# Kernel tuning notes

Hardware: AMD Instinct MI355X
Metric: run time of the kernel (lower is better)

The kernel has to match this reference:

```python
import jax, jax.numpy as jnp
import numpy as np

N_NODES = 50000
N_EDGES = 800000
F_IN = 128
HID = 256
K = 5
N_GRAPHS = 64


def setup_inputs() -> dict:
    key = jax.random.key(0)
    ks = jax.random.split(key, 16)
    x = jax.random.normal(ks[0], (N_NODES, F_IN), dtype=jnp.float32)
    edge_index = jax.random.randint(ks[1], (2, N_EDGES), 0, N_NODES, dtype=jnp.int32)
    edge_weight = jax.random.uniform(ks[2], (N_EDGES,), dtype=jnp.float32)
    batch = jnp.sort(jax.random.randint(ks[3], (N_NODES,), 0, N_GRAPHS, dtype=jnp.int32))
    s = 0.05
    W1 = jax.random.normal(ks[4], (K, F_IN, HID), dtype=jnp.float32) * s
    b1 = jnp.zeros((HID,), dtype=jnp.float32)
    W2 = jax.random.normal(ks[5], (K, HID, HID), dtype=jnp.float32) * s
    b2 = jnp.zeros((HID,), dtype=jnp.float32)
    W3 = jax.random.normal(ks[6], (K, HID, HID), dtype=jnp.float32) * s
    b3 = jnp.zeros((HID,), dtype=jnp.float32)
    lw1 = jax.random.normal(ks[7], (HID, HID), dtype=jnp.float32) * s
    lb1 = jnp.zeros((HID,), dtype=jnp.float32)
    lw2 = jax.random.normal(ks[8], (HID, 1), dtype=jnp.float32) * s
    lb2 = jnp.zeros((1,), dtype=jnp.float32)
    return dict(x=x, edge_index=edge_index, edge_weight=edge_weight, batch=batch,
                W1=W1, b1=b1, W2=W2, b2=b2, W3=W3, b3=b3,
                lw1=lw1, lb1=lb1, lw2=lw2, lb2=lb2)


def _lap_weights(edge_index, edge_weight, num_nodes):
    # PyG ChebConv with normalization='sym', lambda_max=2.0:
    # L_hat = 2*L/lambda_max - I = -D^{-1/2} A D^{-1/2} on the off-diagonal,
    # zero diagonal. Degree via scatter on edge_index[0].
    src, dst = edge_index[0], edge_index[1]
    deg = jax.ops.segment_sum(edge_weight, src, num_segments=num_nodes)
    dis = jnp.where(deg > 0, jax.lax.rsqrt(jnp.maximum(deg, 1e-30)), 0.0)
    return -(dis[src] * edge_weight * dis[dst])


def _cheb_conv(x, src, dst, lap_w, W, b):
    # propagate: gather from src, weight, scatter-add to dst
    n = x.shape[0]
    prop = lambda z: jax.ops.segment_sum(lap_w[:, None] * z[src], dst, num_segments=n)
    Tx0 = x
    out = Tx0 @ W[0]
    Tx1 = prop(x)
    out = out + Tx1 @ W[1]
    for k in range(2, W.shape[0]):
        Tx2 = 2.0 * prop(Tx1) - Tx0
        out = out + Tx2 @ W[k]
        Tx0, Tx1 = Tx1, Tx2
    return out + b


def reference(x, edge_index, edge_weight, batch, W1, b1, W2, b2, W3, b3, lw1, lb1, lw2, lb2):
    src, dst = edge_index[0], edge_index[1]
    lap_w = _lap_weights(edge_index, edge_weight, x.shape[0])
    h = jax.nn.relu(_cheb_conv(x, src, dst, lap_w, W1, b1))
    h = _cheb_conv(h, src, dst, lap_w, W2, b2)
    h = jax.nn.relu(_cheb_conv(h, src, dst, lap_w, W3, b3))
    # global mean pool over graphs in the batch
    sums = jax.ops.segment_sum(h, batch, num_segments=N_GRAPHS)
    cnts = jax.ops.segment_sum(jnp.ones((h.shape[0],), h.dtype), batch, num_segments=N_GRAPHS)
    g = sums / jnp.maximum(cnts, 1.0)[:, None]
    g = jax.nn.relu(g)  # dropout is identity in eval mode
    g = g @ lw1 + lb1
    g = g @ lw2 + lb2
    return jax.nn.sigmoid(g)
```

## Files before the change

### kernel.cpp

```cpp
#include <hip/hip_runtime.h>
#include <math.h>

typedef unsigned int uint;
typedef unsigned short ushort;
typedef __bf16 bf16x8 __attribute__((ext_vector_type(8)));
typedef float f32x4 __attribute__((ext_vector_type(4)));
typedef __attribute__((address_space(1))) const void gvoid;
typedef __attribute__((address_space(3))) void svoid;

__device__ __forceinline__ float b2f(ushort u) {
  uint v = ((uint)u) << 16;
  return __uint_as_float(v);
}
__device__ __forceinline__ ushort f2b(float f) {
  uint u = __float_as_uint(f);
  u += 0x7FFFu + ((u >> 16) & 1u);
  return (ushort)(u >> 16);
}
__device__ __forceinline__ uint pack2(float a, float b) {
  return (uint)f2b(a) | ((uint)f2b(b) << 16);
}


__global__ void edge_kernel(const int* __restrict__ src, const int* __restrict__ dst,
                            const float* __restrict__ w, float* __restrict__ degp,
                            int* __restrict__ cntp, int ne, int nb) {
  int e = blockIdx.x * blockDim.x + threadIdx.x;
  if (e < ne) {
    int part = blockIdx.x & 7;
    atomicAdd(&degp[(size_t)part * nb + src[e]], w[e]);
    atomicAdd(&cntp[(size_t)part * nb + dst[e]], 1);
  }
}

__global__ __launch_bounds__(256) void node_kernel(const float* __restrict__ degp,
                                                   const int* __restrict__ cntp,
                                                   float* __restrict__ dis,
                                                   int* __restrict__ rowstart,
                                                   int* __restrict__ rowcnt,
                                                   int* __restrict__ cursor,
                                                   int* __restrict__ total,
                                                   const int* __restrict__ batch,
                                                   int nb, int ng, int* __restrict__ bnd) {
  __shared__ int ls[256];
  __shared__ int base;
  int tid = threadIdx.x;
  int i = blockIdx.x * 256 + tid;
  int c = 0;
  float d = 0.f;
  if (i < nb) {
#pragma unroll
    for (int p = 0; p < 8; ++p) {
      c += cntp[(size_t)p * nb + i];
      d += degp[(size_t)p * nb + i];
    }
  }
  ls[tid] = c;
  __syncthreads();
  for (int off = 1; off < 256; off <<= 1) {
    int v = (tid >= off) ? ls[tid - off] : 0;
    __syncthreads();
    ls[tid] += v;
    __syncthreads();
  }
  if (tid == 255) base = atomicAdd(total, ls[255]);
  __syncthreads();
  if (i < nb) {
    int pos = base + ls[tid] - c;
    rowstart[i] = pos;
    cursor[i] = pos;
    rowcnt[i] = c;
    dis[i] = d > 0.f ? rsqrtf(fmaxf(d, 1e-30f)) : 0.f;
  }
  if (blockIdx.x == 0 && tid <= ng) {
    int lo = 0, hi = nb;
    while (lo < hi) {
      int mid = (lo + hi) >> 1;
      if (batch[mid] < tid) lo = mid + 1; else hi = mid;
    }
    bnd[tid] = lo;
  }
}

__global__ void scatter_kernel(const int* __restrict__ src, const int* __restrict__ dst,
                               const float* __restrict__ w, const float* __restrict__ dis,
                               int* __restrict__ cursor, int2* __restrict__ cv, int ne) {
  int e = blockIdx.x * blockDim.x + threadIdx.x;
  if (e < ne) {
    int d = dst[e], s = src[e];
    int pos = atomicAdd(&cursor[d], 1);
    float v = -(dis[s] * w[e] * dis[d]);
    cv[pos] = make_int2(s, __float_as_int(v));
  }
}


__global__ void xcvt_kernel(const float* __restrict__ x, uint* __restrict__ o, int total) {
  int i = blockIdx.x * blockDim.x + threadIdx.x;
  if (i < total) {
    float2 v = *(const float2*)(x + (size_t)i * 2);
    o[i] = pack2(v.x, v.y);
  }
}

__global__ void wprep_kernel(const float* __restrict__ W, ushort* __restrict__ WT,
                             int shift, int Ktot, int total) {
  int id = blockIdx.x * blockDim.x + threadIdx.x;
  if (id >= total) return;
  int n = id / Ktot;
  int k = id - n * Ktot;
  int fin = k & ((1 << shift) - 1);
  int ord = k >> shift;
  WT[id] = f2b(W[(size_t)(ord << shift) * 256 + (size_t)fin * 256 + n]);
}

__global__ void wprep2_kernel(const float* __restrict__ W2, ushort* __restrict__ WT2,
                              const float* __restrict__ W3, ushort* __restrict__ WT3,
                              int tot) {
  int id = blockIdx.x * blockDim.x + threadIdx.x;
  if (id >= 2 * tot) return;
  const float* W = (id < tot) ? W2 : W3;
  ushort* WT = (id < tot) ? WT2 : WT3;
  int t = (id < tot) ? id : id - tot;
  int n = t / 1280;
  int k = t - n * 1280;
  int fin = k & 255;
  int ord = k >> 8;
  WT[t] = f2b(W[(size_t)(ord << 8) * 256 + (size_t)fin * 256 + n]);
}


#define RFL __builtin_amdgcn_readfirstlane

template <int WIDE>
__global__ __launch_bounds__(256) void spmm_wave(const int* __restrict__ rowstart,
                                                 const int* __restrict__ rowcnt,
                                                 const int2* __restrict__ cv,
                                                 const uint* __restrict__ X,
                                                 uint* __restrict__ out,
                                                 const uint* __restrict__ sub,
                                                 float alpha, int nb) {
  int row = blockIdx.x * 4 + (threadIdx.x >> 6);
  if (row >= nb) return;
  int lane = threadIdx.x & 63;
  int e0 = RFL(rowstart[row]);
  int cnt = RFL(rowcnt[row]);
  int e1 = e0 + cnt;
  float a0 = 0.f, a1 = 0.f, a2 = 0.f, a3 = 0.f;
  int e = e0;
  if (WIDE) {
    const uint2* Xr = (const uint2*)X;
    for (; e + 4 <= e1; e += 4) {
      int2 p0 = cv[e], p1 = cv[e + 1], p2 = cv[e + 2], p3 = cv[e + 3];
      int c0 = RFL(p0.x); float v0 = __uint_as_float(RFL((uint)p0.y));
      int c1 = RFL(p1.x); float v1 = __uint_as_float(RFL((uint)p1.y));
      int c2 = RFL(p2.x); float v2 = __uint_as_float(RFL((uint)p2.y));
      int c3 = RFL(p3.x); float v3 = __uint_as_float(RFL((uint)p3.y));
      uint2 g0 = Xr[(size_t)c0 * 64 + lane];
      uint2 g1 = Xr[(size_t)c1 * 64 + lane];
      uint2 g2 = Xr[(size_t)c2 * 64 + lane];
      uint2 g3 = Xr[(size_t)c3 * 64 + lane];
      a0 = fmaf(v0, b2f((ushort)(g0.x & 0xFFFF)), a0);
      a1 = fmaf(v0, b2f((ushort)(g0.x >> 16)), a1);
      a2 = fmaf(v0, b2f((ushort)(g0.y & 0xFFFF)), a2);
      a3 = fmaf(v0, b2f((ushort)(g0.y >> 16)), a3);
      a0 = fmaf(v1, b2f((ushort)(g1.x & 0xFFFF)), a0);
      a1 = fmaf(v1, b2f((ushort)(g1.x >> 16)), a1);
      a2 = fmaf(v1, b2f((ushort)(g1.y & 0xFFFF)), a2);
      a3 = fmaf(v1, b2f((ushort)(g1.y >> 16)), a3);
      a0 = fmaf(v2, b2f((ushort)(g2.x & 0xFFFF)), a0);
      a1 = fmaf(v2, b2f((ushort)(g2.x >> 16)), a1);
      a2 = fmaf(v2, b2f((ushort)(g2.y & 0xFFFF)), a2);
      a3 = fmaf(v2, b2f((ushort)(g2.y >> 16)), a3);
      a0 = fmaf(v3, b2f((ushort)(g3.x & 0xFFFF)), a0);
      a1 = fmaf(v3, b2f((ushort)(g3.x >> 16)), a1);
      a2 = fmaf(v3, b2f((ushort)(g3.y & 0xFFFF)), a2);
      a3 = fmaf(v3, b2f((ushort)(g3.y >> 16)), a3);
    }
    for (; e < e1; ++e) {
      int2 p0 = cv[e];
      int c0 = RFL(p0.x); float v0 = __uint_as_float(RFL((uint)p0.y));
      uint2 g0 = Xr[(size_t)c0 * 64 + lane];
      a0 = fmaf(v0, b2f((ushort)(g0.x & 0xFFFF)), a0);
      a1 = fmaf(v0, b2f((ushort)(g0.x >> 16)), a1);
      a2 = fmaf(v0, b2f((ushort)(g0.y & 0xFFFF)), a2);
      a3 = fmaf(v0, b2f((ushort)(g0.y >> 16)), a3);
    }
    float r0 = alpha * a0, r1 = alpha * a1, r2 = alpha * a2, r3 = alpha * a3;
    if (sub) {
      uint2 s = ((const uint2*)sub)[(size_t)row * 64 + lane];
      r0 -= b2f((ushort)(s.x & 0xFFFF));
      r1 -= b2f((ushort)(s.x >> 16));
      r2 -= b2f((ushort)(s.y & 0xFFFF));
      r3 -= b2f((ushort)(s.y >> 16));
    }
    ((uint2*)out)[(size_t)row * 64 + lane] = make_uint2(pack2(r0, r1), pack2(r2, r3));
  } else {
    for (; e + 4 <= e1; e += 4) {
      int2 p0 = cv[e], p1 = cv[e + 1], p2 = cv[e + 2], p3 = cv[e + 3];
      int c0 = RFL(p0.x); float v0 = __uint_as_float(RFL((uint)p0.y));
      int c1 = RFL(p1.x); float v1 = __uint_as_float(RFL((uint)p1.y));
      int c2 = RFL(p2.x); float v2 = __uint_as_float(RFL((uint)p2.y));
      int c3 = RFL(p3.x); float v3 = __uint_as_float(RFL((uint)p3.y));
      uint g0 = X[(size_t)c0 * 64 + lane];
      uint g1 = X[(size_t)c1 * 64 + lane];
      uint g2 = X[(size_t)c2 * 64 + lane];
      uint g3 = X[(size_t)c3 * 64 + lane];
      a0 = fmaf(v0, b2f((ushort)(g0 & 0xFFFF)), a0);
      a1 = fmaf(v0, b2f((ushort)(g0 >> 16)), a1);
      a0 = fmaf(v1, b2f((ushort)(g1 & 0xFFFF)), a0);
      a1 = fmaf(v1, b2f((ushort)(g1 >> 16)), a1);
      a0 = fmaf(v2, b2f((ushort)(g2 & 0xFFFF)), a0);
      a1 = fmaf(v2, b2f((ushort)(g2 >> 16)), a1);
      a0 = fmaf(v3, b2f((ushort)(g3 & 0xFFFF)), a0);
      a1 = fmaf(v3, b2f((ushort)(g3 >> 16)), a1);
    }
    for (; e < e1; ++e) {
      int2 p0 = cv[e];
      int c0 = RFL(p0.x); float v0 = __uint_as_float(RFL((uint)p0.y));
      uint g0 = X[(size_t)c0 * 64 + lane];
      a0 = fmaf(v0, b2f((ushort)(g0 & 0xFFFF)), a0);
      a1 = fmaf(v0, b2f((ushort)(g0 >> 16)), a1);
    }
    float r0 = alpha * a0, r1 = alpha * a1;
    if (sub) {
      uint s = sub[(size_t)row * 64 + lane];
      r0 -= b2f((ushort)(s & 0xFFFF));
      r1 -= b2f((ushort)(s >> 16));
    }
    out[(size_t)row * 64 + lane] = pack2(r0, r1);
  }
}


struct APtrs { const ushort* p[5]; };

template <int RELU, int SHIFT>
__global__ __launch_bounds__(256, 2) void gemm_mfma(APtrs ap, const ushort* __restrict__ WT,
                                                    const float* __restrict__ bias,
                                                    ushort* __restrict__ C, int M, int Ktot) {
  constexpr int LDA = 1 << SHIFT;
  __shared__ __align__(16) char lAb[16384];
  __shared__ __align__(16) char lBb[16384];
  int tid = threadIdx.x;
  int lane = tid & 63, w = tid >> 6;
  int wr = w >> 1, wc = w & 1;
  int row0 = blockIdx.x * 128, col0 = blockIdx.y * 128;

  f32x4 acc[4][4];
#pragma unroll
  for (int i = 0; i < 4; ++i)
#pragma unroll
    for (int n = 0; n < 4; ++n) acc[i][n] = {0.f, 0.f, 0.f, 0.f};

  for (int k0 = 0; k0 < Ktot; k0 += 64) {
    const ushort* Ab = ap.p[k0 >> SHIFT];
    int ka = k0 & (LDA - 1);
    __syncthreads();
#pragma unroll
    for (int c = 0; c < 4; ++c) {
      int base = c * 4096 + w * 1024;
      int off = base + lane * 16;
      int row = off >> 7, within = off & 127;
      int lw = within ^ ((row & 7) << 4);
      int grow = row0 + row; if (grow >= M) grow = M - 1;
      const ushort* g = Ab + (size_t)grow * LDA + ka + (lw >> 1);
      __builtin_amdgcn_global_load_lds((gvoid*)g, (svoid*)(lAb + base), 16, 0, 0);
    }
#pragma unroll
    for (int c = 0; c < 4; ++c) {
      int base = c * 4096 + w * 1024;
      int off = base + lane * 16;
      int n = off >> 7, within = off & 127;
      int lw = within ^ ((n & 7) << 4);
      const ushort* g = WT + (size_t)(col0 + n) * Ktot + k0 + (lw >> 1);
      __builtin_amdgcn_global_load_lds((gvoid*)g, (svoid*)(lBb + base), 16, 0, 0);
    }
    asm volatile("s_waitcnt vmcnt(0)" ::: "memory");
    __syncthreads();
#pragma unroll
    for (int s = 0; s < 2; ++s) {
      int kb = (s << 6) + ((lane >> 4) << 4);
      bf16x8 af[4], bfr[4];
#pragma unroll
      for (int i = 0; i < 4; ++i) {
        int mrow = (wr << 6) + (i << 4) + (lane & 15);
        af[i] = *(const bf16x8*)(lAb + (mrow << 7) + (kb ^ ((mrow & 7) << 4)));
      }
#pragma unroll
      for (int n = 0; n < 4; ++n) {
        int ncol = (wc << 6) + (n << 4) + (lane & 15);
        bfr[n] = *(const bf16x8*)(lBb + (ncol << 7) + (kb ^ ((ncol & 7) << 4)));
      }
#pragma unroll
      for (int i = 0; i < 4; ++i)
#pragma unroll
        for (int n = 0; n < 4; ++n)
          acc[i][n] = __builtin_amdgcn_mfma_f32_16x16x32_bf16(af[i], bfr[n], acc[i][n], 0, 0, 0);
    }
  }
  int cb = col0 + (wc << 6) + (lane & 15);
  float bv[4];
#pragma unroll
  for (int n = 0; n < 4; ++n) bv[n] = bias[cb + (n << 4)];
#pragma unroll
  for (int i = 0; i < 4; ++i) {
    int rbase = row0 + (wr << 6) + (i << 4) + ((lane >> 4) << 2);
#pragma unroll
    for (int r = 0; r < 4; ++r) {
      int row = rbase + r;
      if (row < M) {
#pragma unroll
        for (int n = 0; n < 4; ++n) {
          float v = acc[i][n][r] + bv[n];
          if (RELU) v = fmaxf(v, 0.f);
          C[(size_t)row * 256 + cb + (n << 4)] = f2b(v);
        }
      }
    }
  }
}


__global__ __launch_bounds__(256) void head_kernel(const uint* __restrict__ h,
                                                   const int* __restrict__ bnd,
                                                   const float* __restrict__ lw1,
                                                   const float* __restrict__ lb1,
                                                   const float* __restrict__ lw2,
                                                   const float* __restrict__ lb2,
                                                   float* __restrict__ out) {
  int g = blockIdx.x;
  int j = threadIdx.x;
  __shared__ float gs[256];
  __shared__ float red[256];
  int s = bnd[g], e = bnd[g + 1];
  int ui = j >> 1, half = j & 1;
  float acc = 0.f;
  int i = s;
  for (; i + 4 <= e; i += 4) {
    uint p0 = h[(size_t)(i + 0) * 128 + ui];
    uint p1 = h[(size_t)(i + 1) * 128 + ui];
    uint p2 = h[(size_t)(i + 2) * 128 + ui];
    uint p3 = h[(size_t)(i + 3) * 128 + ui];
    acc += b2f((ushort)(half ? (p0 >> 16) : (p0 & 0xFFFF)));
    acc += b2f((ushort)(half ? (p1 >> 16) : (p1 & 0xFFFF)));
    acc += b2f((ushort)(half ? (p2 >> 16) : (p2 & 0xFFFF)));
    acc += b2f((ushort)(half ? (p3 >> 16) : (p3 & 0xFFFF)));
  }
  for (; i < e; ++i) {
    uint p = h[(size_t)i * 128 + ui];
    acc += b2f((ushort)(half ? (p >> 16) : (p & 0xFFFF)));
  }
  float c = fmaxf((float)(e - s), 1.f);
  gs[j] = fmaxf(acc / c, 0.f);
  __syncthreads();
  float t = lb1[j];
  for (int k = 0; k < 256; ++k) t = fmaf(gs[k], lw1[k * 256 + j], t);
  red[j] = t * lw2[j];
  __syncthreads();
  for (int off = 128; off > 0; off >>= 1) {
    if (j < off) red[j] += red[j + off];
    __syncthreads();
  }
  if (j == 0) out[g] = 1.f / (1.f + expf(-(red[0] + lb2[0])));
}


extern "C" void kernel_launch(void* const* d_in, const int* in_sizes, int n_in,
                              void* d_out, int out_size, void* d_ws, size_t ws_size,
                              hipStream_t stream) {
  const float* x    = (const float*)d_in[0];
  const int*   ei   = (const int*)d_in[1];
  const float* ew   = (const float*)d_in[2];
  const int*   batch= (const int*)d_in[3];
  const float* W1 = (const float*)d_in[4];
  const float* b1 = (const float*)d_in[5];
  const float* W2 = (const float*)d_in[6];
  const float* b2 = (const float*)d_in[7];
  const float* W3 = (const float*)d_in[8];
  const float* b3 = (const float*)d_in[9];
  const float* lw1 = (const float*)d_in[10];
  const float* lb1 = (const float*)d_in[11];
  const float* lw2 = (const float*)d_in[12];
  const float* lb2 = (const float*)d_in[13];
  float* out = (float*)d_out;

  const int NE  = in_sizes[2];
  const int NB  = in_sizes[3];
  const int FIN = in_sizes[0] / NB;
  const int NG  = out_size;
  const int* src = ei;
  const int* dst = ei + NE;

  char* p = (char*)d_ws;
  auto alloc = [&](size_t bytes) {
    char* q = p;
    p += (bytes + 255) & ~(size_t)255;
    return q;
  };
  char* zb = (char*)alloc((size_t)(16 * NB + 1) * 4);
  float* degp = (float*)zb;
  int*   cntp = (int*)(zb + (size_t)8 * NB * 4);
  int*   total= (int*)(zb + (size_t)16 * NB * 4);
  float* dis      = (float*)alloc((size_t)NB * 4);
  int*   rowstart = (int*)alloc((size_t)NB * 4);
  int*   rowcnt   = (int*)alloc((size_t)NB * 4);
  int*   cursor   = (int*)alloc((size_t)NB * 4);
  int2*  cv       = (int2*)alloc((size_t)NE * 8);
  int*   bnd      = (int*)alloc((size_t)(NG + 1) * 4);
  uint*  X0  = (uint*)alloc((size_t)NB * (FIN / 2) * 4);
  uint*  T1  = (uint*)alloc((size_t)NB * 128 * 4);
  uint*  T2  = (uint*)alloc((size_t)NB * 128 * 4);
  uint*  T3  = (uint*)alloc((size_t)NB * 128 * 4);
  uint*  T4  = (uint*)alloc((size_t)NB * 128 * 4);
  uint*  HA  = (uint*)alloc((size_t)NB * 128 * 4);
  uint*  HB  = (uint*)alloc((size_t)NB * 128 * 4);
  ushort* WT1 = (ushort*)alloc((size_t)256 * 5 * FIN * 2);
  ushort* WT2 = (ushort*)alloc((size_t)256 * 5 * 256 * 2);
  ushort* WT3 = (ushort*)alloc((size_t)256 * 5 * 256 * 2);

  hipMemsetAsync(zb, 0, (size_t)(16 * NB + 1) * 4, stream);

  int eb = (NE + 255) / 256;
  int nbb = (NB + 255) / 256;
  edge_kernel<<<eb, 256, 0, stream>>>(src, dst, ew, degp, cntp, NE, NB);
  node_kernel<<<nbb, 256, 0, stream>>>(degp, cntp, dis, rowstart, rowcnt, cursor, total,
                                       batch, NB, NG, bnd);
  scatter_kernel<<<eb, 256, 0, stream>>>(src, dst, ew, dis, cursor, cv, NE);

  int xcnt = NB * (FIN / 2);
  xcvt_kernel<<<(xcnt + 255) / 256, 256, 0, stream>>>(x, X0, xcnt);
  {
    int kt1 = 5 * FIN, tot1 = 256 * kt1;
    wprep_kernel<<<(tot1 + 255) / 256, 256, 0, stream>>>(W1, WT1, 7, kt1, tot1);
    int tot2 = 256 * 1280;
    wprep2_kernel<<<(2 * tot2 + 255) / 256, 256, 0, stream>>>(W2, WT2, W3, WT3, tot2);
  }

  int sgrid = (NB + 3) / 4;
  dim3 ggrid((NB + 127) / 128, 2);

  spmm_wave<0><<<sgrid, 256, 0, stream>>>(rowstart, rowcnt, cv, X0, T1, nullptr, 1.f, NB);
  spmm_wave<0><<<sgrid, 256, 0, stream>>>(rowstart, rowcnt, cv, T1, T2, X0, 2.f, NB);
  spmm_wave<0><<<sgrid, 256, 0, stream>>>(rowstart, rowcnt, cv, T2, T3, T1, 2.f, NB);
  spmm_wave<0><<<sgrid, 256, 0, stream>>>(rowstart, rowcnt, cv, T3, T4, T2, 2.f, NB);
  {
    APtrs ap = {{(const ushort*)X0, (const ushort*)T1, (const ushort*)T2,
                 (const ushort*)T3, (const ushort*)T4}};
    gemm_mfma<1, 7><<<ggrid, 256, 0, stream>>>(ap, WT1, b1, (ushort*)HA, NB, 5 * FIN);
  }
  spmm_wave<1><<<sgrid, 256, 0, stream>>>(rowstart, rowcnt, cv, HA, T1, nullptr, 1.f, NB);
  spmm_wave<1><<<sgrid, 256, 0, stream>>>(rowstart, rowcnt, cv, T1, T2, HA, 2.f, NB);
  spmm_wave<1><<<sgrid, 256, 0, stream>>>(rowstart, rowcnt, cv, T2, T3, T1, 2.f, NB);
  spmm_wave<1><<<sgrid, 256, 0, stream>>>(rowstart, rowcnt, cv, T3, T4, T2, 2.f, NB);
  {
    APtrs ap = {{(const ushort*)HA, (const ushort*)T1, (const ushort*)T2,
                 (const ushort*)T3, (const ushort*)T4}};
    gemm_mfma<0, 8><<<ggrid, 256, 0, stream>>>(ap, WT2, b2, (ushort*)HB, NB, 5 * 256);
  }
  spmm_wave<1><<<sgrid, 256, 0, stream>>>(rowstart, rowcnt, cv, HB, T1, nullptr, 1.f, NB);
  spmm_wave<1><<<sgrid, 256, 0, stream>>>(rowstart, rowcnt, cv, T1, T2, HB, 2.f, NB);
  spmm_wave<1><<<sgrid, 256, 0, stream>>>(rowstart, rowcnt, cv, T2, T3, T1, 2.f, NB);
  spmm_wave<1><<<sgrid, 256, 0, stream>>>(rowstart, rowcnt, cv, T3, T4, T2, 2.f, NB);
  {
    APtrs ap = {{(const ushort*)HB, (const ushort*)T1, (const ushort*)T2,
                 (const ushort*)T3, (const ushort*)T4}};
    gemm_mfma<1, 8><<<ggrid, 256, 0, stream>>>(ap, WT3, b3, (ushort*)HA, NB, 5 * 256);
  }

  head_kernel<<<NG, 256, 0, stream>>>(HA, bnd, lw1, lb1, lw2, lb2, out);
}
```

Before: 1.012 ms.

## Widen GEMM tile to full output width and fuse prep kernels

The MFMA GEMM now computes all 256 output columns per block instead of splitting columns across two blocks. Each A tile is then loaded from global memory once instead of twice, at the cost of doubled accumulator registers, a larger LDS B buffer and half as many blocks. The input conversion and three weight-transpose kernels are merged into a single prep launch to cut launch overhead.

```diff
diff --git a/kernel.cpp b/kernel.cpp
--- a/kernel.cpp
+++ b/kernel.cpp
@@ -95,33 +95,32 @@
 }
 
 
-__global__ void xcvt_kernel(const float* __restrict__ x, uint* __restrict__ o, int total) {
-  int i = blockIdx.x * blockDim.x + threadIdx.x;
-  if (i < total) {
-    float2 v = *(const float2*)(x + (size_t)i * 2);
-    o[i] = pack2(v.x, v.y);
-  }
-}
-
-__global__ void wprep_kernel(const float* __restrict__ W, ushort* __restrict__ WT,
-                             int shift, int Ktot, int total) {
+__global__ void prep_kernel(const float* __restrict__ x, uint* __restrict__ X0,
+                            const float* __restrict__ W1, ushort* __restrict__ WT1,
+                            const float* __restrict__ W2, ushort* __restrict__ WT2,
+                            const float* __restrict__ W3, ushort* __restrict__ WT3,
+                            int xcnt, int tot1, int tot2) {
   int id = blockIdx.x * blockDim.x + threadIdx.x;
-  if (id >= total) return;
-  int n = id / Ktot;
-  int k = id - n * Ktot;
-  int fin = k & ((1 << shift) - 1);
-  int ord = k >> shift;
-  WT[id] = f2b(W[(size_t)(ord << shift) * 256 + (size_t)fin * 256 + n]);
-}
-
-__global__ void wprep2_kernel(const float* __restrict__ W2, ushort* __restrict__ WT2,
-                              const float* __restrict__ W3, ushort* __restrict__ WT3,
-                              int tot) {
-  int id = blockIdx.x * blockDim.x + threadIdx.x;
-  if (id >= 2 * tot) return;
-  const float* W = (id < tot) ? W2 : W3;
-  ushort* WT = (id < tot) ? WT2 : WT3;
-  int t = (id < tot) ? id : id - tot;
+  if (id < xcnt) {
+    float2 v = *(const float2*)(x + (size_t)id * 2);
+    X0[id] = pack2(v.x, v.y);
+    return;
+  }
+  id -= xcnt;
+  if (id < tot1) {
+    int kt1 = tot1 >> 8;
+    int n = id / kt1;
+    int k = id - n * kt1;
+    int fin = k & ((kt1 / 5) - 1);
+    int ord = k / (kt1 / 5);
+    WT1[id] = f2b(W1[(size_t)ord * (kt1 / 5) * 256 + (size_t)fin * 256 + n]);
+    return;
+  }
+  id -= tot1;
+  if (id >= 2 * tot2) return;
+  const float* W = (id < tot2) ? W2 : W3;
+  ushort* WT = (id < tot2) ? WT2 : WT3;
+  int t = (id < tot2) ? id : id - tot2;
   int n = t / 1280;
   int k = t - n * 1280;
   int fin = k & 255;
@@ -241,17 +240,17 @@
                                                     ushort* __restrict__ C, int M, int Ktot) {
   constexpr int LDA = 1 << SHIFT;
   __shared__ __align__(16) char lAb[16384];
-  __shared__ __align__(16) char lBb[16384];
+  __shared__ __align__(16) char lBb[32768];
   int tid = threadIdx.x;
   int lane = tid & 63, w = tid >> 6;
   int wr = w >> 1, wc = w & 1;
-  int row0 = blockIdx.x * 128, col0 = blockIdx.y * 128;
-
-  f32x4 acc[4][4];
+  int row0 = blockIdx.x * 128;
+
+  f32x4 acc[4][8];
 #pragma unroll
   for (int i = 0; i < 4; ++i)
 #pragma unroll
-    for (int n = 0; n < 4; ++n) acc[i][n] = {0.f, 0.f, 0.f, 0.f};
+    for (int n = 0; n < 8; ++n) acc[i][n] = {0.f, 0.f, 0.f, 0.f};
 
   for (int k0 = 0; k0 < Ktot; k0 += 64) {
     const ushort* Ab = ap.p[k0 >> SHIFT];
@@ -268,12 +267,12 @@
       __builtin_amdgcn_global_load_lds((gvoid*)g, (svoid*)(lAb + base), 16, 0, 0);
     }
 #pragma unroll
-    for (int c = 0; c < 4; ++c) {
+    for (int c = 0; c < 8; ++c) {
       int base = c * 4096 + w * 1024;
       int off = base + lane * 16;
       int n = off >> 7, within = off & 127;
       int lw = within ^ ((n & 7) << 4);
-      const ushort* g = WT + (size_t)(col0 + n) * Ktot + k0 + (lw >> 1);
+      const ushort* g = WT + (size_t)n * Ktot + k0 + (lw >> 1);
       __builtin_amdgcn_global_load_lds((gvoid*)g, (svoid*)(lBb + base), 16, 0, 0);
     }
     asm volatile("s_waitcnt vmcnt(0)" ::: "memory");
@@ -281,28 +280,28 @@
 #pragma unroll
     for (int s = 0; s < 2; ++s) {
       int kb = (s << 6) + ((lane >> 4) << 4);
-      bf16x8 af[4], bfr[4];
+      bf16x8 af[4], bfr[8];
 #pragma unroll
       for (int i = 0; i < 4; ++i) {
         int mrow = (wr << 6) + (i << 4) + (lane & 15);
         af[i] = *(const bf16x8*)(lAb + (mrow << 7) + (kb ^ ((mrow & 7) << 4)));
       }
 #pragma unroll
-      for (int n = 0; n < 4; ++n) {
-        int ncol = (wc << 6) + (n << 4) + (lane & 15);
+      for (int n = 0; n < 8; ++n) {
+        int ncol = (wc << 7) + (n << 4) + (lane & 15);
         bfr[n] = *(const bf16x8*)(lBb + (ncol << 7) + (kb ^ ((ncol & 7) << 4)));
       }
 #pragma unroll
       for (int i = 0; i < 4; ++i)
 #pragma unroll
-        for (int n = 0; n < 4; ++n)
+        for (int n = 0; n < 8; ++n)
           acc[i][n] = __builtin_amdgcn_mfma_f32_16x16x32_bf16(af[i], bfr[n], acc[i][n], 0, 0, 0);
     }
   }
-  int cb = col0 + (wc << 6) + (lane & 15);
-  float bv[4];
-#pragma unroll
-  for (int n = 0; n < 4; ++n) bv[n] = bias[cb + (n << 4)];
+  int cb0 = (wc << 7) + (lane & 15);
+  float bv[8];
+#pragma unroll
+  for (int n = 0; n < 8; ++n) bv[n] = bias[cb0 + (n << 4)];
 #pragma unroll
   for (int i = 0; i < 4; ++i) {
     int rbase = row0 + (wr << 6) + (i << 4) + ((lane >> 4) << 2);
@@ -311,10 +310,10 @@
       int row = rbase + r;
       if (row < M) {
 #pragma unroll
-        for (int n = 0; n < 4; ++n) {
+        for (int n = 0; n < 8; ++n) {
           float v = acc[i][n][r] + bv[n];
           if (RELU) v = fmaxf(v, 0.f);
-          C[(size_t)row * 256 + cb + (n << 4)] = f2b(v);
+          C[(size_t)row * 256 + cb0 + (n << 4)] = f2b(v);
         }
       }
     }
@@ -428,17 +427,17 @@
                                        batch, NB, NG, bnd);
   scatter_kernel<<<eb, 256, 0, stream>>>(src, dst, ew, dis, cursor, cv, NE);
 
-  int xcnt = NB * (FIN / 2);
-  xcvt_kernel<<<(xcnt + 255) / 256, 256, 0, stream>>>(x, X0, xcnt);
   {
-    int kt1 = 5 * FIN, tot1 = 256 * kt1;
-    wprep_kernel<<<(tot1 + 255) / 256, 256, 0, stream>>>(W1, WT1, 7, kt1, tot1);
+    int xcnt = NB * (FIN / 2);
+    int tot1 = 256 * 5 * FIN;
     int tot2 = 256 * 1280;
-    wprep2_kernel<<<(2 * tot2 + 255) / 256, 256, 0, stream>>>(W2, WT2, W3, WT3, tot2);
+    int ptot = xcnt + tot1 + 2 * tot2;
+    prep_kernel<<<(ptot + 255) / 256, 256, 0, stream>>>(x, X0, W1, WT1, W2, WT2, W3, WT3,
+                                                        xcnt, tot1, tot2);
   }
 
   int sgrid = (NB + 3) / 4;
-  dim3 ggrid((NB + 127) / 128, 2);
+  int ggrid = (NB + 127) / 128;
 
   spmm_wave<0><<<sgrid, 256, 0, stream>>>(rowstart, rowcnt, cv, X0, T1, nullptr, 1.f, NB);
   spmm_wave<0><<<sgrid, 256, 0, stream>>>(rowstart, rowcnt, cv, T1, T2, X0, 2.f, NB);
```

Result: faster. 991.7 us (-2.0%).
